# Performance work log

Hardware: AMD Instinct MI355X
Metric: run time of the kernel (lower is better)

## Reference

```python
import jax, jax.numpy as jnp
import numpy as np

MAX_WAVELENGTH = 10000
BIG_NEG = -2.3819763e38

def _rope(x, positions):
    # x: [B, L, H, D], positions: [B, L] float32
    d = x.shape[-1]
    freq_exp = 2.0 / d * jnp.arange(d // 2, dtype=jnp.float32)
    timescale = MAX_WAVELENGTH ** freq_exp
    radians = (positions[..., None] / timescale[None, None, :])[..., None, :]  # [B,L,1,D/2]
    sin, cos = jnp.sin(radians), jnp.cos(radians)
    x1, x2 = jnp.split(x, 2, axis=-1)
    return jnp.concatenate([x1 * cos - x2 * sin, x2 * cos + x1 * sin], axis=-1).astype(x.dtype)

def _adaln_rmsnorm(x, cond, Wmod, bmod):
    # RMSNorm in fp32, then AdaLN scale/shift; returns (normed, gate[B,1,D])
    var = jnp.mean(jnp.square(x.astype(jnp.float32)), axis=-1, keepdims=True)
    normed = x * jax.lax.rsqrt(var + 1e-6)
    mod = (cond @ Wmod + bmod)[:, None, :]  # [B,1,3D]
    scale, shift, gate = jnp.split(mod, 3, axis=-1)
    return (normed * (1 + scale) + shift).astype(x.dtype), gate

def setup_inputs() -> dict:
    key = jax.random.key(0)
    ks = jax.random.split(key, 9)
    B, T, D, F, N, K, H = 2, 2048, 2048, 16384, 8, 1, 256
    x = jax.random.normal(ks[0], (B, T, D), jnp.float32)
    positions = jnp.broadcast_to(jnp.arange(T, dtype=jnp.float32), (B, T))
    attn_mask = jnp.broadcast_to(jnp.tril(jnp.ones((T, T), dtype=bool))[None, None], (B, 1, T, T))
    cond = jax.random.normal(ks[1], (B, D), jnp.float32)
    Wmod_a = jax.random.normal(ks[2], (D, 3 * D), jnp.float32) * 0.02
    bmod_a = jnp.zeros((3 * D,), jnp.float32)
    Wq = jax.random.normal(ks[3], (N, D, H), jnp.float32) * (D ** -0.5)
    Wkv = jax.random.normal(ks[4], (2, K, D, H), jnp.float32) * (D ** -0.5)
    Wo = jax.random.normal(ks[5], (N, H, D), jnp.float32) * ((N * H) ** -0.5)
    Wmod_f = jax.random.normal(ks[6], (D, 3 * D), jnp.float32) * 0.02
    bmod_f = jnp.zeros((3 * D,), jnp.float32)
    Wg = jax.random.normal(ks[7], (2, D, F), jnp.float32) * (D ** -0.5)
    Wl = jax.random.normal(ks[8], (F, D), jnp.float32) * (F ** -0.5)
    return dict(x=x, positions=positions, attn_mask=attn_mask, cond=cond,
                Wmod_a=Wmod_a, bmod_a=bmod_a, Wq=Wq, Wkv=Wkv, Wo=Wo,
                Wmod_f=Wmod_f, bmod_f=bmod_f, Wg=Wg, Wl=Wl)

def reference(x, positions, attn_mask, cond, Wmod_a, bmod_a, Wq, Wkv, Wo, Wmod_f, bmod_f, Wg, Wl):
    K = Wkv.shape[1]               # num_kv_heads
    H = Wq.shape[-1]               # head_dim
    # --- pre-attention AdaLN RMSNorm ---
    n, gate_a = _adaln_rmsnorm(x, cond, Wmod_a, bmod_a)
    # --- GQA projections ---
    q = jnp.einsum('BTD,NDH->BTNH', n, Wq)
    k = jnp.einsum('BSD,KDH->BSKH', n, Wkv[0])
    v = jnp.einsum('BSD,KDH->BSKH', n, Wkv[1])
    q = _rope(q, positions) * (H ** -0.5)
    k = _rope(k, positions)
    B, T, N, _ = q.shape
    q = q.reshape(B, T, K, N // K, H)  # B T K G H
    logits = jnp.einsum('BTKGH,BSKH->BKGTS', q, k, preferred_element_type=jnp.float32)
    masked = jnp.where(attn_mask[:, :, None, :, :], logits, BIG_NEG)
    probs = jax.nn.softmax(masked, axis=-1).astype(x.dtype)
    enc = jnp.einsum('BKGTS,BSKH->BTKGH', probs, v).reshape(B, T, N, H)
    attn_out = jnp.einsum('BTNH,NHD->BTD', enc, Wo)
    # gated residual
    x = x + attn_out * gate_a
    # --- pre-FFN AdaLN RMSNorm + gated-GeLU MLP ---
    n, gate_f = _adaln_rmsnorm(x, cond, Wmod_f, bmod_f)
    h = jax.nn.gelu(jnp.einsum('BTD,DF->BTF', n, Wg[0])) * jnp.einsum('BTD,DF->BTF', n, Wg[1])
    mlp_out = jnp.einsum('BTF,FD->BTD', h, Wl)
    return x + mlp_out * gate_f
```

## Files before the change

kernel.cpp:

```cpp
#include <hip/hip_runtime.h>
#include <hip/hip_bf16.h>

typedef __bf16 bf16_t;
typedef __bf16 bf16x8 __attribute__((ext_vector_type(8)));
typedef float  f32x4  __attribute__((ext_vector_type(4)));

#define DEV static __device__ __forceinline__

DEV void gload16(const bf16_t* g, bf16_t* l) {
    __builtin_amdgcn_global_load_lds(
        (const __attribute__((address_space(1))) void*)g,
        (__attribute__((address_space(3))) void*)l, 16, 0, 0);
}

enum { EPI_F32 = 0, EPI_BF16 = 1, EPI_RES = 2, EPI_GELU = 3, EPI_MUL = 4 };

#define G_MFMA(d, a, b) d = __builtin_amdgcn_mfma_f32_16x16x32_bf16(a, b, d, 0, 0, 0)

#define COMPUTE(AB0, AB1, BB0, BB1)                                           \
  { bf16x8 aF[8], bF[4];                                                      \
    _Pragma("unroll") for (int m8 = 0; m8 < 8; m8++)                          \
      aF[m8] = *(const bf16x8*)(AB0 + (m8 >> 2) * 4096 + (m8 & 3) * 1024);    \
    _Pragma("unroll") for (int nj = 0; nj < 4; nj++)                          \
      bF[nj] = *(const bf16x8*)(BB0 + nj * 1024);                             \
    _Pragma("unroll") for (int m8 = 0; m8 < 8; m8++)                          \
      _Pragma("unroll") for (int nj = 0; nj < 4; nj++)                        \
        G_MFMA(acc[m8][nj], aF[m8], bF[nj]);                                  \
    _Pragma("unroll") for (int m8 = 0; m8 < 8; m8++)                          \
      aF[m8] = *(const bf16x8*)(AB1 + (m8 >> 2) * 4096 + (m8 & 3) * 1024);    \
    _Pragma("unroll") for (int nj = 0; nj < 4; nj++)                          \
      bF[nj] = *(const bf16x8*)(BB1 + nj * 1024);                             \
    _Pragma("unroll") for (int m8 = 0; m8 < 8; m8++)                          \
      _Pragma("unroll") for (int nj = 0; nj < 4; nj++)                        \
        G_MFMA(acc[m8][nj], aF[m8], bF[nj]);                                  \
  }

#define STAGE8(kt, bi)                                                        \
  { SCA(kt, bi, 0); SCA(kt, bi, 1); SCA(kt, bi, 2); SCA(kt, bi, 3);           \
    SCB(kt, bi, 0); SCB(kt, bi, 1); SCB(kt, bi, 2); SCB(kt, bi, 3); }

template<int EPI>
__global__ __launch_bounds__(512, 1)
void gemma(const bf16_t* __restrict__ A, const bf16_t* __restrict__ Bt,
           void* __restrict__ Cout, int Kd, int lda, int ldb, int ldc,
           long sCz,
           const float* __restrict__ res, const float* __restrict__ gate,
           int gateStride, int rowsPerB, const bf16_t* __restrict__ aux)
{
    const int nbx = gridDim.x;
    const int nwg = nbx * gridDim.y;
    int lin = blockIdx.y * nbx + blockIdx.x;
    const int q8 = nwg >> 3, r8 = nwg & 7;
    const int xcd = lin & 7, oo = lin >> 3;
    lin = (xcd < r8 ? xcd * (q8 + 1) : r8 * (q8 + 1) + (xcd - r8) * q8) + oo;
    const long m0 = (long)(lin / nbx) * 256;
    const long n0 = (long)(lin % nbx) * 256;
    const long kb = (long)blockIdx.z * Kd;

    const int tid = threadIdx.x;
    const int l   = tid & 63;
    const int w   = tid >> 6;
    const int wr  = w >> 2;
    const int wcn = w & 3;

    __shared__ bf16_t sA[2][16384];
    __shared__ bf16_t sB[2][16384];

    const long sgc = (long)(((l & 7) ^ (l >> 3)) << 3);
    const int NT = Kd >> 6;
    const int NI = NT >> 1;

    const bf16_t* pA0 = A + (m0 + 0 * 64 + w * 8 + (l >> 3)) * (long)lda + kb + sgc;
    const bf16_t* pA1 = A + (m0 + 1 * 64 + w * 8 + (l >> 3)) * (long)lda + kb + sgc;
    const bf16_t* pA2 = A + (m0 + 2 * 64 + w * 8 + (l >> 3)) * (long)lda + kb + sgc;
    const bf16_t* pA3 = A + (m0 + 3 * 64 + w * 8 + (l >> 3)) * (long)lda + kb + sgc;
    const bf16_t* pB0 = Bt + (n0 + 0 * 64 + w * 8 + (l >> 3)) * (long)ldb + kb + sgc;
    const bf16_t* pB1 = Bt + (n0 + 1 * 64 + w * 8 + (l >> 3)) * (long)ldb + kb + sgc;
    const bf16_t* pB2 = Bt + (n0 + 2 * 64 + w * 8 + (l >> 3)) * (long)ldb + kb + sgc;
    const bf16_t* pB3 = Bt + (n0 + 3 * 64 + w * 8 + (l >> 3)) * (long)ldb + kb + sgc;

#define SCA(kt, bi, c) gload16(pA##c + (kt), &sA[bi][(c) * 4096 + w * 512])
#define SCB(kt, bi, c) gload16(pB##c + (kt), &sB[bi][(c) * 4096 + w * 512])

    f32x4 acc[8][4];
#pragma unroll
    for (int i = 0; i < 8; i++)
#pragma unroll
        for (int j = 0; j < 4; j++) acc[i][j] = f32x4{0.f, 0.f, 0.f, 0.f};

    const int co0 = ((l >> 4) ^ (l & 7)) << 3;
    const int co1 = ((4 + (l >> 4)) ^ (l & 7)) << 3;

    const bf16_t* rbA00 = &sA[0][(wr * 128 + (l & 15)) * 64 + co0];
    const bf16_t* rbA01 = &sA[0][(wr * 128 + (l & 15)) * 64 + co1];
    const bf16_t* rbA10 = &sA[1][(wr * 128 + (l & 15)) * 64 + co0];
    const bf16_t* rbA11 = &sA[1][(wr * 128 + (l & 15)) * 64 + co1];
    const bf16_t* rbB00 = &sB[0][(wcn * 64 + (l & 15)) * 64 + co0];
    const bf16_t* rbB01 = &sB[0][(wcn * 64 + (l & 15)) * 64 + co1];
    const bf16_t* rbB10 = &sB[1][(wcn * 64 + (l & 15)) * 64 + co0];
    const bf16_t* rbB11 = &sB[1][(wcn * 64 + (l & 15)) * 64 + co1];

    STAGE8(0, 0);

    for (int it = 0; it < NI; ++it) {
        const int v = 2 * it + 1;
        asm volatile("s_waitcnt lgkmcnt(0)" ::: "memory");
        __builtin_amdgcn_s_barrier();
        STAGE8((long)v * 64, 1);
        asm volatile("s_waitcnt vmcnt(8)" ::: "memory");
        __builtin_amdgcn_s_barrier();
        COMPUTE(rbA00, rbA01, rbB00, rbB01);
        asm volatile("s_waitcnt lgkmcnt(0)" ::: "memory");
        __builtin_amdgcn_s_barrier();
        if (v + 1 < NT) {
            STAGE8((long)(v + 1) * 64, 0);
            asm volatile("s_waitcnt vmcnt(8)" ::: "memory");
        } else {
            asm volatile("s_waitcnt vmcnt(0)" ::: "memory");
        }
        __builtin_amdgcn_s_barrier();
        COMPUTE(rbA10, rbA11, rbB10, rbB11);
    }

#pragma unroll
    for (int mi = 0; mi < 8; mi++) {
#pragma unroll
        for (int nj = 0; nj < 4; nj++) {
            f32x4 vv = acc[mi][nj];
            const long col   = n0 + wcn * 64 + nj * 16 + (l & 15);
            const long row0r = m0 + wr * 128 + mi * 16 + ((l >> 4) * 4);
#pragma unroll
            for (int e = 0; e < 4; e++) {
                const long row = row0r + e;
                const long idx = row * (long)ldc + col + (long)blockIdx.z * sCz;
                const float val = vv[e];
                if constexpr (EPI == EPI_F32) {
                    ((float*)Cout)[idx] = val;
                } else if constexpr (EPI == EPI_BF16) {
                    ((bf16_t*)Cout)[idx] = (bf16_t)val;
                } else if constexpr (EPI == EPI_RES) {
                    const int b = (int)(row / rowsPerB);
                    ((float*)Cout)[idx] = res[row * (long)ldc + col] + val * gate[(long)b * gateStride + col];
                } else if constexpr (EPI == EPI_GELU) {
                    const float gl = 0.5f * val * (1.f + tanhf(0.7978845608f * (val + 0.044715f * val * val * val)));
                    ((bf16_t*)Cout)[idx] = (bf16_t)gl;
                } else if constexpr (EPI == EPI_MUL) {
                    ((bf16_t*)Cout)[idx] = (bf16_t)((float)aux[idx] * val);
                }
            }
        }
    }
#undef SCA
#undef SCB
}

__global__ __launch_bounds__(256)
void combine_splitk(const float* __restrict__ P, const float* __restrict__ res,
                    const float* __restrict__ gate, float* __restrict__ out,
                    int D, int T, int gateStride, long zstride, long n4)
{
    for (long i4 = (long)blockIdx.x * 256 + threadIdx.x; i4 < n4; i4 += (long)gridDim.x * 256) {
        const long i = i4 * 4;
        const float4 p0 = *(const float4*)(P + i);
        const float4 p1 = *(const float4*)(P + i + zstride);
        const float4 xv = *(const float4*)(res + i);
        const long row = i / D;
        const int  b   = (int)(row / T);
        const int  col = (int)(i - row * D);
        const float* gp = gate + (long)b * gateStride + col;
        float4 r;
        r.x = xv.x + (p0.x + p1.x) * gp[0];
        r.y = xv.y + (p0.y + p1.y) * gp[1];
        r.z = xv.z + (p0.z + p1.z) * gp[2];
        r.w = xv.w + (p0.w + p1.w) * gp[3];
        *(float4*)(out + i) = r;
    }
}

template<int EPI, int CAUSAL>
__global__ __launch_bounds__(256)
void gemm_bt(const bf16_t* __restrict__ A, const bf16_t* __restrict__ Bt,
             void* __restrict__ Cout,
             int M, int N, int Kd, int lda, int ldb, int ldc,
             long sAz, long sBz, long sCz,
             const float* __restrict__ res, const float* __restrict__ gate,
             int gateStride, int rowsPerB, const bf16_t* __restrict__ aux)
{
    const int tid = threadIdx.x;
    const int l   = tid & 63;
    const int w   = tid >> 6;
    const int wr  = w >> 1, wc = w & 1;
    const long m0 = (long)blockIdx.y * 128;
    const long n0 = (long)blockIdx.x * 128;
    const int  z  = blockIdx.z;

    if constexpr (CAUSAL == 1) {
        if (n0 > m0 + 127) return;
    }
    int kend = Kd;
    if constexpr (CAUSAL == 2) {
        const int kc = (int)m0 + 128;
        kend = kc < Kd ? kc : Kd;
    }

    A  += (long)z * sAz;
    Bt += (long)z * sBz;

    __shared__ bf16_t As[128 * 32];
    __shared__ bf16_t Bs[128 * 32];

    const int srow = w * 16 + (l >> 2);
    const int scol = (l & 3) * 8;
    const bf16_t* Ag = A  + (m0 + srow) * (long)lda + scol;
    const bf16_t* Bg = Bt + (n0 + srow) * (long)ldb + scol;

    bf16_t* ldsA = As + w * 512;
    bf16_t* ldsB = Bs + w * 512;

    f32x4 acc[16];
    const f32x4 fz = {0.f, 0.f, 0.f, 0.f};
#pragma unroll
    for (int i = 0; i < 16; i++) acc[i] = fz;

    for (int k0 = 0; k0 < kend; k0 += 32) {
        gload16(Ag + k0,                  ldsA);
        gload16(Ag + k0 + 64 * (long)lda, ldsA + 2048);
        gload16(Bg + k0,                  ldsB);
        gload16(Bg + k0 + 64 * (long)ldb, ldsB + 2048);
        __syncthreads();

        bf16x8 af[4], bfr[4];
#pragma unroll
        for (int f = 0; f < 4; f++) {
            af[f]  = *(const bf16x8*)(As + (wr * 64 + f * 16 + (l & 15)) * 32 + (l >> 4) * 8);
            bfr[f] = *(const bf16x8*)(Bs + (wc * 64 + f * 16 + (l & 15)) * 32 + (l >> 4) * 8);
        }
#pragma unroll
        for (int i = 0; i < 4; i++)
#pragma unroll
            for (int j = 0; j < 4; j++)
                acc[i * 4 + j] = __builtin_amdgcn_mfma_f32_16x16x32_bf16(af[i], bfr[j], acc[i * 4 + j], 0, 0, 0);
        __syncthreads();
    }

#pragma unroll
    for (int i = 0; i < 4; i++) {
#pragma unroll
        for (int j = 0; j < 4; j++) {
            f32x4 v = acc[i * 4 + j];
            const long col  = n0 + wc * 64 + j * 16 + (l & 15);
            const long row0 = m0 + wr * 64 + i * 16 + ((l >> 4) * 4);
#pragma unroll
            for (int e = 0; e < 4; e++) {
                const long row = row0 + e;
                const long idx = row * (long)ldc + col + (long)z * sCz;
                const float val = v[e];
                if constexpr (EPI == EPI_F32) {
                    ((float*)Cout)[idx] = val;
                } else if constexpr (EPI == EPI_BF16) {
                    ((bf16_t*)Cout)[idx] = (bf16_t)val;
                } else if constexpr (EPI == EPI_RES) {
                    const int b = (int)(row / rowsPerB);
                    ((float*)Cout)[idx] = res[row * (long)ldc + col] + val * gate[(long)b * gateStride + col];
                } else if constexpr (EPI == EPI_GELU) {
                    const float gl = 0.5f * val * (1.f + tanhf(0.7978845608f * (val + 0.044715f * val * val * val)));
                    ((bf16_t*)Cout)[idx] = (bf16_t)gl;
                } else {
                    ((bf16_t*)Cout)[idx] = (bf16_t)((float)aux[idx] * val);
                }
            }
        }
    }
}

__global__ __launch_bounds__(256)
void transpose_f2b(const float* __restrict__ in, bf16_t* __restrict__ out,
                   int R, int C, long inStride, long outStride)
{
    __shared__ float tile[32][33];
    in  += (long)blockIdx.z * inStride;
    out += (long)blockIdx.z * outStride;
    const int c0 = blockIdx.x * 32, r0 = blockIdx.y * 32;
    const int tx = threadIdx.x, ty = threadIdx.y;
#pragma unroll
    for (int i = 0; i < 4; i++)
        tile[ty + i * 8][tx] = in[(long)(r0 + ty + i * 8) * C + c0 + tx];
    __syncthreads();
#pragma unroll
    for (int i = 0; i < 4; i++)
        out[(long)(c0 + ty + i * 8) * R + r0 + tx] = (bf16_t)tile[tx][ty + i * 8];
}

__global__ __launch_bounds__(256)
void modk_part(const float* __restrict__ cond, const float* __restrict__ W,
               float* __restrict__ part, int D3, int KS)
{
    const int j = blockIdx.x * 256 + threadIdx.x;
    const int b = blockIdx.y;
    const int z = blockIdx.z;
    const float* cb = cond + (long)b * (KS * gridDim.z);
    float s = 0.f;
    const int d0 = z * KS;
#pragma unroll 4
    for (int d = d0; d < d0 + KS; d++) s += cb[d] * W[(long)d * D3 + j];
    part[((long)z * gridDim.y + b) * D3 + j] = s;
}

__global__ __launch_bounds__(256)
void modk_reduce(const float* __restrict__ part, const float* __restrict__ bvec,
                 float* __restrict__ mod, int D3, int NZ)
{
    const int j = blockIdx.x * 256 + threadIdx.x;
    const int b = blockIdx.y;
    float s = bvec[j];
    for (int z = 0; z < NZ; z++) s += part[((long)z * gridDim.y + b) * D3 + j];
    mod[(long)b * D3 + j] = s;
}

__global__ __launch_bounds__(256)
void rmsnorm_adaln(const float* __restrict__ xin, const float* __restrict__ mod,
                   bf16_t* __restrict__ out, int D, int T, int D3)
{
    const long row = blockIdx.x;
    const int  b   = (int)(row / T);
    const int  tid = threadIdx.x;
    const float4* x4 = (const float4*)(xin + row * (long)D);
    const float4 v0 = x4[tid], v1 = x4[tid + 256];
    float ss = v0.x * v0.x + v0.y * v0.y + v0.z * v0.z + v0.w * v0.w
             + v1.x * v1.x + v1.y * v1.y + v1.z * v1.z + v1.w * v1.w;
    for (int o = 32; o; o >>= 1) ss += __shfl_down(ss, o, 64);
    __shared__ float red[4];
    if ((tid & 63) == 0) red[tid >> 6] = ss;
    __syncthreads();
    ss = red[0] + red[1] + red[2] + red[3];
    const float rs = rsqrtf(ss / (float)D + 1e-6f);
    const float* sc = mod + (long)b * D3;
    const float* sh = sc + D;
    const float4 s0 = ((const float4*)sc)[tid], s1 = ((const float4*)sc)[tid + 256];
    const float4 h0 = ((const float4*)sh)[tid], h1 = ((const float4*)sh)[tid + 256];
    bf16_t* orow = out + row * (long)D;
    orow[tid * 4 + 0]         = (bf16_t)(v0.x * rs * (1.f + s0.x) + h0.x);
    orow[tid * 4 + 1]         = (bf16_t)(v0.y * rs * (1.f + s0.y) + h0.y);
    orow[tid * 4 + 2]         = (bf16_t)(v0.z * rs * (1.f + s0.z) + h0.z);
    orow[tid * 4 + 3]         = (bf16_t)(v0.w * rs * (1.f + s0.w) + h0.w);
    orow[(tid + 256) * 4 + 0] = (bf16_t)(v1.x * rs * (1.f + s1.x) + h1.x);
    orow[(tid + 256) * 4 + 1] = (bf16_t)(v1.y * rs * (1.f + s1.y) + h1.y);
    orow[(tid + 256) * 4 + 2] = (bf16_t)(v1.z * rs * (1.f + s1.z) + h1.z);
    orow[(tid + 256) * 4 + 3] = (bf16_t)(v1.w * rs * (1.f + s1.w) + h1.w);
}

__global__ __launch_bounds__(128)
void rope_q(const bf16_t* __restrict__ qp, const float* __restrict__ positions,
            bf16_t* __restrict__ qo, int T, int ldq, int H)
{
    const int t = blockIdx.x, n = blockIdx.y, b = blockIdx.z;
    const int i = threadIdx.x;
    const long in0 = ((long)(b * T + t)) * ldq + n * H;
    const float x1 = (float)qp[in0 + i];
    const float x2 = (float)qp[in0 + i + 128];
    const float pos = positions[b * T + t];
    const float inv = expf(-9.210340371976184f * (float)i / 128.f);
    float s, c;
    sincosf(pos * inv, &s, &c);
    const float scl = 0.0625f;
    const long out0 = (((long)(b * 8 + n)) * T + t) * H;
    qo[out0 + i]       = (bf16_t)((x1 * c - x2 * s) * scl);
    qo[out0 + i + 128] = (bf16_t)((x2 * c + x1 * s) * scl);
}

__global__ __launch_bounds__(128)
void rope_kv(const bf16_t* __restrict__ kvp, const float* __restrict__ positions,
             bf16_t* __restrict__ ko, bf16_t* __restrict__ vt, int T, int H, int S, int ldkv)
{
    const int t = blockIdx.x, b = blockIdx.y;
    const int i = threadIdx.x;
    const long in0 = ((long)(b * T + t)) * ldkv;
    const float k1 = (float)kvp[in0 + i];
    const float k2 = (float)kvp[in0 + i + 128];
    const float pos = positions[b * T + t];
    const float inv = expf(-9.210340371976184f * (float)i / 128.f);
    float s, c;
    sincosf(pos * inv, &s, &c);
    const long ko0 = ((long)(b * T + t)) * H;
    ko[ko0 + i]       = (bf16_t)(k1 * c - k2 * s);
    ko[ko0 + i + 128] = (bf16_t)(k2 * c + k1 * s);
    vt[((long)b * H + i) * S + t]       = kvp[in0 + 256 + i];
    vt[((long)b * H + i + 128) * S + t] = kvp[in0 + 256 + i + 128];
}

__global__ __launch_bounds__(256)
void softmax_causal(const float* __restrict__ sc, bf16_t* __restrict__ pr, int T, int S)
{
    const int t = blockIdx.x, g = blockIdx.y;
    const long row = (long)g * T + t;
    const float* srow = sc + row * S;
    bf16_t* prow = pr + row * S;
    const int tid = threadIdx.x;
    const int limit = t | 127;
    const int nch = (limit >> 8) + 1;
    float vals[8];
    float mx = -3.4e38f;
    for (int i = 0; i < nch; i++) {
        const int s = i * 256 + tid;
        const float v = (s <= t) ? srow[s] : -3.4e38f;
        vals[i] = v;
        mx = fmaxf(mx, v);
    }
    for (int o = 32; o; o >>= 1) mx = fmaxf(mx, __shfl_down(mx, o, 64));
    __shared__ float red[4];
    if ((tid & 63) == 0) red[tid >> 6] = mx;
    __syncthreads();
    mx = fmaxf(fmaxf(red[0], red[1]), fmaxf(red[2], red[3]));
    __syncthreads();
    float sum = 0.f;
    for (int i = 0; i < nch; i++) {
        const int s = i * 256 + tid;
        const float e = (s <= t) ? __expf(vals[i] - mx) : 0.f;
        vals[i] = e;
        sum += e;
    }
    for (int o = 32; o; o >>= 1) sum += __shfl_down(sum, o, 64);
    if ((tid & 63) == 0) red[tid >> 6] = sum;
    __syncthreads();
    sum = red[0] + red[1] + red[2] + red[3];
    const float invs = 1.f / sum;
    for (int i = 0; i < nch; i++)
        prow[i * 256 + tid] = (bf16_t)(vals[i] * invs);
}

extern "C" void kernel_launch(void* const* d_in, const int* in_sizes, int n_in,
                              void* d_out, int out_size, void* d_ws, size_t ws_size,
                              hipStream_t stream)
{
    const float* x      = (const float*)d_in[0];
    const float* pos    = (const float*)d_in[1];
    const float* cond   = (const float*)d_in[3];
    const float* Wmod_a = (const float*)d_in[4];
    const float* bmod_a = (const float*)d_in[5];
    const float* Wq     = (const float*)d_in[6];
    const float* Wkv    = (const float*)d_in[7];
    const float* Wo     = (const float*)d_in[8];
    const float* Wmod_f = (const float*)d_in[9];
    const float* bmod_f = (const float*)d_in[10];
    const float* Wg     = (const float*)d_in[11];
    const float* Wl     = (const float*)d_in[12];

    constexpr int  Bb = 2, T = 2048, D = 2048, F = 16384, Nh = 8, H = 256;
    constexpr int  NH = 2048, S = 2048, G = 8, BT = 4096, D3 = 6144;
    constexpr int  KSLICE = 64, NZ = D / KSLICE;
    constexpr int  NQKV = 2560;

    char* ws = (char*)d_ws;
    size_t off = 0;
    auto alloc = [&](size_t bytes) { char* p = ws + off; off += bytes; return p; };

    bf16_t* WQT  = (bf16_t*)alloc((size_t)NH * D * 2);
    bf16_t* WKVT = (bf16_t*)alloc((size_t)512 * D * 2);
    bf16_t* WOT  = (bf16_t*)alloc((size_t)D * NH * 2);
    bf16_t* WGT  = (bf16_t*)alloc((size_t)2 * F * D * 2);
    bf16_t* WLT  = (bf16_t*)alloc((size_t)D * F * 2);
    float*  MODA = (float*)alloc((size_t)Bb * D3 * 4);
    float*  MODF = (float*)alloc((size_t)Bb * D3 * 4);
    float*  PART = (float*)alloc((size_t)NZ * Bb * D3 * 4);
    bf16_t* NA   = (bf16_t*)alloc((size_t)BT * D * 2);
    bf16_t* QKVP = (bf16_t*)alloc((size_t)BT * NQKV * 2);
    bf16_t* Qr   = (bf16_t*)alloc((size_t)Bb * Nh * T * H * 2);
    bf16_t* Kr   = (bf16_t*)alloc((size_t)Bb * T * H * 2);
    bf16_t* VT   = (bf16_t*)alloc((size_t)Bb * H * S * 2);
    bf16_t* ENC  = (bf16_t*)alloc((size_t)BT * NH * 2);
    float*  X1   = (float*)alloc((size_t)BT * D * 4);
    bf16_t* NF   = (bf16_t*)alloc((size_t)BT * D * 2);
    const size_t scBytes = (size_t)G * T * S * 4;
    const size_t prBytes = (size_t)G * T * S * 2;
    const size_t hBytes  = (size_t)BT * F * 2;
    const size_t bigBytes = (scBytes + prBytes > hBytes) ? (scBytes + prBytes) : hBytes;
    char* big = alloc(bigBytes);
    float*  SC = (float*)big;
    bf16_t* PR = (bf16_t*)(big + scBytes);
    bf16_t* Hb = (bf16_t*)big;
    float*  PARTK = (float*)(big + hBytes);
    (void)ws_size; (void)in_sizes; (void)n_in; (void)out_size;

    const dim3 tb(32, 8);
    transpose_f2b<<<dim3(H / 32, D / 32, 8), tb, 0, stream>>>(Wq,  WQT,  D,  H, (long)D * H, (long)H * D);
    transpose_f2b<<<dim3(H / 32, D / 32, 2), tb, 0, stream>>>(Wkv, WKVT, D,  H, (long)D * H, (long)H * D);
    transpose_f2b<<<dim3(D / 32, NH / 32, 1), tb, 0, stream>>>(Wo, WOT, NH,  D, 0, 0);
    transpose_f2b<<<dim3(F / 32, D / 32, 2), tb, 0, stream>>>(Wg,  WGT,  D,  F, (long)D * F, (long)F * D);
    transpose_f2b<<<dim3(D / 32, F / 32, 1), tb, 0, stream>>>(Wl,  WLT,  F,  D, 0, 0);
    modk_part<<<dim3(D3 / 256, Bb, NZ), 256, 0, stream>>>(cond, Wmod_a, PART, D3, KSLICE);
    modk_reduce<<<dim3(D3 / 256, Bb), 256, 0, stream>>>(PART, bmod_a, MODA, D3, NZ);
    modk_part<<<dim3(D3 / 256, Bb, NZ), 256, 0, stream>>>(cond, Wmod_f, PART, D3, KSLICE);
    modk_reduce<<<dim3(D3 / 256, Bb), 256, 0, stream>>>(PART, bmod_f, MODF, D3, NZ);
    rmsnorm_adaln<<<BT, 256, 0, stream>>>(x, MODA, NA, D, T, D3);
    gemma<EPI_BF16><<<dim3(NQKV / 256, BT / 256, 1), 512, 0, stream>>>(
        NA, WQT, QKVP, D, D, D, NQKV, 0, nullptr, nullptr, 0, 0, nullptr);
    rope_q<<<dim3(T, Nh, Bb), 128, 0, stream>>>(QKVP, pos, Qr, T, NQKV, H);
    rope_kv<<<dim3(T, Bb), 128, 0, stream>>>(QKVP + NH, pos, Kr, VT, T, H, S, NQKV);
    for (int b = 0; b < Bb; b++) {
        gemm_bt<EPI_F32, 1><<<dim3(S / 128, T / 128, G), 256, 0, stream>>>(
            Qr + (long)b * Nh * T * H, Kr + (long)b * T * H, SC,
            T, S, H, H, H, S, (long)T * H, 0, (long)T * S, nullptr, nullptr, 0, 0, nullptr);
        softmax_causal<<<dim3(T, G), 256, 0, stream>>>(SC, PR, T, S);
        gemm_bt<EPI_BF16, 2><<<dim3(H / 128, T / 128, G), 256, 0, stream>>>(
            PR, VT + (long)b * H * S, ENC + (long)b * T * NH,
            T, H, S, S, S, NH, (long)T * S, 0, (long)H, nullptr, nullptr, 0, 0, nullptr);
    }
    gemma<EPI_F32><<<dim3(D / 256, BT / 256, 2), 512, 0, stream>>>(
        ENC, WOT, PARTK, NH / 2, NH, NH, D, (long)BT * D, nullptr, nullptr, 0, 0, nullptr);
    combine_splitk<<<2048, 256, 0, stream>>>(
        PARTK, x, MODA + 2 * D, X1, D, T, D3, (long)BT * D, (long)BT * D / 4);
    rmsnorm_adaln<<<BT, 256, 0, stream>>>(X1, MODF, NF, D, T, D3);
    gemma<EPI_GELU><<<dim3(F / 256, BT / 256, 1), 512, 0, stream>>>(
        NF, WGT, Hb, D, D, D, F, 0, nullptr, nullptr, 0, 0, nullptr);
    gemma<EPI_MUL><<<dim3(F / 256, BT / 256, 1), 512, 0, stream>>>(
        NF, WGT + (long)F * D, Hb, D, D, D, F, 0, nullptr, nullptr, 0, 0, Hb);
    gemma<EPI_F32><<<dim3(D / 256, BT / 256, 2), 512, 0, stream>>>(
        Hb, WLT, PARTK, F / 2, F, F, D, (long)BT * D, nullptr, nullptr, 0, 0, nullptr);
    combine_splitk<<<2048, 256, 0, stream>>>(
        PARTK, X1, MODF + 2 * D, (float*)d_out, D, T, D3, (long)BT * D, (long)BT * D / 4);
}
```

Before: 1.526 ms.

## Batch attention across both batches and store scores in bf16 in place

The per-batch loop of three attention launches becomes one launch per stage covering all 16 head-batch pairs, with z split into batch and head for the K/V and output offsets. Attention scores are now written as bf16 instead of fp32, and softmax overwrites them in place, removing the separate probability buffer. This cuts score write and read traffic and kernel launches, and gives each launch more blocks. The cost is rounding the logits to bf16 before softmax, which loses some precision.

```diff
diff --git a/kernel.cpp b/kernel.cpp
--- a/kernel.cpp
+++ b/kernel.cpp
@@ -182,9 +182,7 @@
 void gemm_bt(const bf16_t* __restrict__ A, const bf16_t* __restrict__ Bt,
              void* __restrict__ Cout,
              int M, int N, int Kd, int lda, int ldb, int ldc,
-             long sAz, long sBz, long sCz,
-             const float* __restrict__ res, const float* __restrict__ gate,
-             int gateStride, int rowsPerB, const bf16_t* __restrict__ aux)
+             long sAz, long sBz, long sCz, long sCz2)
 {
     const int tid = threadIdx.x;
     const int l   = tid & 63;
@@ -204,7 +202,8 @@
     }
 
     A  += (long)z * sAz;
-    Bt += (long)z * sBz;
+    Bt += (long)(z >> 3) * sBz;
+    const long cOff = (long)(z >> 3) * sCz2 + (long)(z & 7) * sCz;
 
     __shared__ bf16_t As[128 * 32];
     __shared__ bf16_t Bs[128 * 32];
@@ -253,21 +252,8 @@
 #pragma unroll
             for (int e = 0; e < 4; e++) {
                 const long row = row0 + e;
-                const long idx = row * (long)ldc + col + (long)z * sCz;
-                const float val = v[e];
-                if constexpr (EPI == EPI_F32) {
-                    ((float*)Cout)[idx] = val;
-                } else if constexpr (EPI == EPI_BF16) {
-                    ((bf16_t*)Cout)[idx] = (bf16_t)val;
-                } else if constexpr (EPI == EPI_RES) {
-                    const int b = (int)(row / rowsPerB);
-                    ((float*)Cout)[idx] = res[row * (long)ldc + col] + val * gate[(long)b * gateStride + col];
-                } else if constexpr (EPI == EPI_GELU) {
-                    const float gl = 0.5f * val * (1.f + tanhf(0.7978845608f * (val + 0.044715f * val * val * val)));
-                    ((bf16_t*)Cout)[idx] = (bf16_t)gl;
-                } else {
-                    ((bf16_t*)Cout)[idx] = (bf16_t)((float)aux[idx] * val);
-                }
+                const long idx = row * (long)ldc + col + cOff;
+                ((bf16_t*)Cout)[idx] = (bf16_t)v[e];
             }
         }
     }
@@ -389,12 +375,11 @@
 }
 
 __global__ __launch_bounds__(256)
-void softmax_causal(const float* __restrict__ sc, bf16_t* __restrict__ pr, int T, int S)
-{
-    const int t = blockIdx.x, g = blockIdx.y;
-    const long row = (long)g * T + t;
-    const float* srow = sc + row * S;
-    bf16_t* prow = pr + row * S;
+void softmax_causal(bf16_t* __restrict__ sc, int T, int S)
+{
+    const int t = blockIdx.x, z = blockIdx.y;
+    const long row = (long)z * T + t;
+    bf16_t* srow = sc + row * S;
     const int tid = threadIdx.x;
     const int limit = t | 127;
     const int nch = (limit >> 8) + 1;
@@ -402,7 +387,7 @@
     float mx = -3.4e38f;
     for (int i = 0; i < nch; i++) {
         const int s = i * 256 + tid;
-        const float v = (s <= t) ? srow[s] : -3.4e38f;
+        const float v = (s <= t) ? (float)srow[s] : -3.4e38f;
         vals[i] = v;
         mx = fmaxf(mx, v);
     }
@@ -425,7 +410,7 @@
     sum = red[0] + red[1] + red[2] + red[3];
     const float invs = 1.f / sum;
     for (int i = 0; i < nch; i++)
-        prow[i * 256 + tid] = (bf16_t)(vals[i] * invs);
+        srow[i * 256 + tid] = (bf16_t)(vals[i] * invs);
 }
 
 extern "C" void kernel_launch(void* const* d_in, const int* in_sizes, int n_in,
@@ -446,7 +431,7 @@
     const float* Wl     = (const float*)d_in[12];
 
     constexpr int  Bb = 2, T = 2048, D = 2048, F = 16384, Nh = 8, H = 256;
-    constexpr int  NH = 2048, S = 2048, G = 8, BT = 4096, D3 = 6144;
+    constexpr int  NH = 2048, S = 2048, BT = 4096, D3 = 6144;
     constexpr int  KSLICE = 64, NZ = D / KSLICE;
     constexpr int  NQKV = 2560;
 
@@ -470,15 +455,13 @@
     bf16_t* ENC  = (bf16_t*)alloc((size_t)BT * NH * 2);
     float*  X1   = (float*)alloc((size_t)BT * D * 4);
     bf16_t* NF   = (bf16_t*)alloc((size_t)BT * D * 2);
-    const size_t scBytes = (size_t)G * T * S * 4;
-    const size_t prBytes = (size_t)G * T * S * 2;
+    const size_t scBytes = (size_t)16 * T * S * 2;
     const size_t hBytes  = (size_t)BT * F * 2;
-    const size_t bigBytes = (scBytes + prBytes > hBytes) ? (scBytes + prBytes) : hBytes;
-    char* big = alloc(bigBytes);
-    float*  SC = (float*)big;
-    bf16_t* PR = (bf16_t*)(big + scBytes);
-    bf16_t* Hb = (bf16_t*)big;
-    float*  PARTK = (float*)(big + hBytes);
+    const size_t headBytes = (scBytes > hBytes) ? scBytes : hBytes;
+    char* big = alloc(headBytes + (size_t)2 * BT * D * 4);
+    bf16_t* SCb   = (bf16_t*)big;
+    bf16_t* Hb    = (bf16_t*)big;
+    float*  PARTK = (float*)(big + headBytes);
     (void)ws_size; (void)in_sizes; (void)n_in; (void)out_size;
 
     const dim3 tb(32, 8);
@@ -496,15 +479,13 @@
         NA, WQT, QKVP, D, D, D, NQKV, 0, nullptr, nullptr, 0, 0, nullptr);
     rope_q<<<dim3(T, Nh, Bb), 128, 0, stream>>>(QKVP, pos, Qr, T, NQKV, H);
     rope_kv<<<dim3(T, Bb), 128, 0, stream>>>(QKVP + NH, pos, Kr, VT, T, H, S, NQKV);
-    for (int b = 0; b < Bb; b++) {
-        gemm_bt<EPI_F32, 1><<<dim3(S / 128, T / 128, G), 256, 0, stream>>>(
-            Qr + (long)b * Nh * T * H, Kr + (long)b * T * H, SC,
-            T, S, H, H, H, S, (long)T * H, 0, (long)T * S, nullptr, nullptr, 0, 0, nullptr);
-        softmax_causal<<<dim3(T, G), 256, 0, stream>>>(SC, PR, T, S);
-        gemm_bt<EPI_BF16, 2><<<dim3(H / 128, T / 128, G), 256, 0, stream>>>(
-            PR, VT + (long)b * H * S, ENC + (long)b * T * NH,
-            T, H, S, S, S, NH, (long)T * S, 0, (long)H, nullptr, nullptr, 0, 0, nullptr);
-    }
+    gemm_bt<EPI_BF16, 1><<<dim3(S / 128, T / 128, 16), 256, 0, stream>>>(
+        Qr, Kr, SCb, T, S, H, H, H, S,
+        (long)T * H, (long)T * H, (long)T * S, 8L * T * S);
+    softmax_causal<<<dim3(T, 16), 256, 0, stream>>>(SCb, T, S);
+    gemm_bt<EPI_BF16, 2><<<dim3(H / 128, T / 128, 16), 256, 0, stream>>>(
+        SCb, VT, ENC, T, H, S, S, S, NH,
+        (long)T * S, (long)H * S, (long)H, (long)T * NH);
     gemma<EPI_F32><<<dim3(D / 256, BT / 256, 2), 512, 0, stream>>>(
         ENC, WOT, PARTK, NH / 2, NH, NH, D, (long)BT * D, nullptr, nullptr, 0, 0, nullptr);
     combine_splitk<<<2048, 256, 0, stream>>>(
```

Result: faster. 1.470 ms, median of 2 (-3.6%).
